# Kernel tuning notes

Measured on AMD Instinct MI355X. Metric: run time of the kernel, lower is better.

The kernel has to match this reference:

```python
import jax, jax.numpy as jnp
import numpy as np

KH, KW = 5, 5
STRIDE = 1
OUT_CH = 32
IN_CH = 3

def setup_inputs() -> dict:
    key = jax.random.key(0)
    x = jax.random.uniform(key, (16, IN_CH, 128, 128), dtype=jnp.float32)
    # reset_parameters: linspace(1, 0, out_channels) repeated over 3 channels
    rgb_weight = jnp.repeat(jnp.linspace(1.0, 0.0, OUT_CH, dtype=jnp.float32)[:, None], IN_CH, axis=1)
    return {"x": x, "rgb_weight": rgb_weight}

def _window_sum(x, kh, kw, s):
    # sum over each (kh, kw) VALID window per channel -> (B, C, oh, ow)
    return jax.lax.reduce_window(x, 0.0, jax.lax.add,
                                 (1, 1, kh, kw), (1, 1, s, s), 'VALID')

def reference(x, rgb_weight):
    kh, kw, s = KH, KW, STRIDE
    K = float(kh * kw)
    s1 = _window_sum(x, kh, kw, s)          # sum x   over window, (B,C,oh,ow)
    s2 = _window_sum(x * x, kh, kw, s)      # sum x^2 over window, (B,C,oh,ow)
    wT = rgb_weight.T                        # (C, O)
    # ||window - w*ones||^2 = S2 - 2*w*S1 + K*w^2 ; per-channel L2 dist summed over channels
    inner = (s2[:, :, None] - 2.0 * wT[None, :, :, None, None] * s1[:, :, None]
             + K * (wT * wT)[None, :, :, None, None])     # (B,C,O,oh,ow)
    dist = jnp.sqrt(jnp.maximum(inner, 0.0)).sum(axis=1)  # (B,O,oh,ow)
    # torch.std(dist) per pixel: unbiased std over all B*O entries of that pixel's dist matrix
    B, O = dist.shape[0], dist.shape[1]
    n = B * O
    mean = dist.mean(axis=(0, 1), keepdims=True)
    std = jnp.sqrt(((dist - mean) ** 2).sum(axis=(0, 1), keepdims=True) / (n - 1))
    # gaussian RBF
    return jnp.exp(-0.5 * (dist / std) ** 2)
```

## Files before the change

### kernel.cpp

```cpp
#include <hip/hip_runtime.h>
#include <math.h>

#define BB 16
#define CC 3
#define OO 32
#define HH 128
#define WW 128
#define OH 124
#define OW 124
#define NPIX (OH * OW)
#define NG   (NPIX / 4)
#define GW   (OW / 4)
#define KF 25.0f

#define TPB  256
#define NBLK (NG / 4)

typedef float vfloat4 __attribute__((ext_vector_type(4)));

#if defined(__has_builtin)
#if __has_builtin(__builtin_amdgcn_sqrtf)
#define FSQRT(x) __builtin_amdgcn_sqrtf(x)
#else
#define FSQRT(x) sqrtf(x)
#endif
#else
#define FSQRT(x) sqrtf(x)
#endif

__global__ __launch_bounds__(TPB, 4)
void fused_one(const float* __restrict__ x,
               const float* __restrict__ wgt,
               float* __restrict__ out) {
    __shared__ float  sS1[BB * CC][17];
    __shared__ float  sS2[BB * CC][17];
    __shared__ float  sPS[BB * 4][17];
    __shared__ float  sPQ[BB * 4][17];
    __shared__ float  sW[OO * CC];
    __shared__ float  sInv[16];
    __shared__ double sRm[16][4];
    __shared__ double sRq[16][4];

    const int t = threadIdx.x;

    const int orig = blockIdx.x;
    const int xcd  = orig & 7;
    const int loc  = orig >> 3;
    const int chunk = ((xcd == 0) ? 0 : 121 + (xcd - 1) * 120) + loc;
    const int g0 = chunk * 4;

    if (t < OO * CC) sW[t] = wgt[t];
    if (t < BB * CC * 4) {
        int bc = t >> 2;
        int p4 = t & 3;
        int g  = g0 + p4;
        int i  = g / GW;
        int j0 = (g % GW) * 4;
        const float* img = x + (size_t)bc * (HH * WW);
        float S1[4] = {0, 0, 0, 0}, S2[4] = {0, 0, 0, 0};
#pragma unroll
        for (int di = 0; di < 5; ++di) {
            const float4* rp = reinterpret_cast<const float4*>(img + (i + di) * WW + j0);
            float4 lo = rp[0], hi = rp[1];
            float v[8] = {lo.x, lo.y, lo.z, lo.w, hi.x, hi.y, hi.z, hi.w};
            float q[8];
#pragma unroll
            for (int k = 0; k < 8; ++k) q[k] = v[k] * v[k];
            float r  = v[0] + v[1] + v[2] + v[3] + v[4];
            float rq = q[0] + q[1] + q[2] + q[3] + q[4];
            S1[0] += r;  S2[0] += rq;
#pragma unroll
            for (int u = 1; u < 4; ++u) {
                r  += v[u + 4] - v[u - 1];
                rq += q[u + 4] - q[u - 1];
                S1[u] += r;  S2[u] += rq;
            }
        }
#pragma unroll
        for (int u = 0; u < 4; ++u) {
            sS1[bc][p4 * 4 + u] = S1[u];
            sS2[bc][p4 * 4 + u] = S2[u];
        }
    }
    __syncthreads();

    const int b  = t >> 4;
    const int og = (t >> 2) & 3;
    const int p4 = t & 3;

    float S1c[CC][4], S2c[CC][4];
#pragma unroll
    for (int c = 0; c < CC; ++c) {
#pragma unroll
        for (int u = 0; u < 4; ++u) {
            S1c[c][u] = sS1[b * CC + c][p4 * 4 + u];
            S2c[c][u] = sS2[b * CC + c][p4 * 4 + u];
        }
    }

    float dist[8][4];
    float sum[4] = {0, 0, 0, 0}, sq[4] = {0, 0, 0, 0};
#pragma unroll
    for (int oo = 0; oo < 8; ++oo) {
        int o = og * 8 + oo;
        float d[4] = {0, 0, 0, 0};
#pragma unroll
        for (int c = 0; c < CC; ++c) {
            float w  = sW[o * CC + c];
            float tw = 2.0f * w;
            float kw = KF * w * w;
#pragma unroll
            for (int u = 0; u < 4; ++u) {
                float inner = S2c[c][u] - tw * S1c[c][u] + kw;
                d[u] += FSQRT(fmaxf(inner, 0.0f));
            }
        }
#pragma unroll
        for (int u = 0; u < 4; ++u) {
            dist[oo][u] = d[u];
            sum[u] += d[u];
            sq[u]  += d[u] * d[u];
        }
    }
#pragma unroll
    for (int u = 0; u < 4; ++u) {
        sPS[b * 4 + og][p4 * 4 + u] = sum[u];
        sPQ[b * 4 + og][p4 * 4 + u] = sq[u];
    }
    __syncthreads();

    if (t < 64) {
        int pix = t >> 2;
        int seg = t & 3;
        double sm = 0.0, sQ = 0.0;
#pragma unroll
        for (int k = 0; k < 16; ++k) {
            sm += (double)sPS[seg * 16 + k][pix];
            sQ += (double)sPQ[seg * 16 + k][pix];
        }
        sRm[pix][seg] = sm;
        sRq[pix][seg] = sQ;
    }
    __syncthreads();
    if (t < 16) {
        double sm = sRm[t][0] + sRm[t][1] + sRm[t][2] + sRm[t][3];
        double sQ = sRq[t][0] + sRq[t][1] + sRq[t][2] + sRq[t][3];
        const double n = (double)(BB * OO);
        double mean = sm / n;
        double var = (sQ - n * mean * mean) / (n - 1.0);
        if (var < 0.0) var = 0.0;
        sInv[t] = (float)(1.0 / sqrt(var));
    }
    __syncthreads();

    float isd[4];
#pragma unroll
    for (int u = 0; u < 4; ++u) isd[u] = sInv[p4 * 4 + u];
    const size_t pixbase = (size_t)(g0 + p4) * 4;

#pragma unroll
    for (int oo = 0; oo < 8; ++oo) {
        int o = og * 8 + oo;
        vfloat4 r;
        float z0 = dist[oo][0] * isd[0]; r.x = __expf(-0.5f * z0 * z0);
        float z1 = dist[oo][1] * isd[1]; r.y = __expf(-0.5f * z1 * z1);
        float z2 = dist[oo][2] * isd[2]; r.z = __expf(-0.5f * z2 * z2);
        float z3 = dist[oo][3] * isd[3]; r.w = __expf(-0.5f * z3 * z3);
        __builtin_nontemporal_store(r,
            reinterpret_cast<vfloat4*>(&out[(size_t)(b * OO + o) * NPIX + pixbase]));
    }
}

extern "C" void kernel_launch(void* const* d_in, const int* in_sizes, int n_in,
                              void* d_out, int out_size, void* d_ws, size_t ws_size,
                              hipStream_t stream) {
    const float* x   = (const float*)d_in[0];
    const float* wgt = (const float*)d_in[1];
    float* out = (float*)d_out;

    fused_one<<<NBLK, TPB, 0, stream>>>(x, wgt, out);
}
```

Baseline: 17.61 us.

## Double pixels per block, fold exp scaling into exp2, drop nontemporal stores

Each block now covers 32 pixels with 512 threads instead of 16 pixels with 256, so there are about half as many blocks. The XCD chunk mapping is rebuilt for the new count, and out-of-range groups are zero-filled and their stores skipped. The Gaussian is now computed as exp2 of minus z squared, with the constant sqrt(0.5*log2 e) folded into the inverse std, which saves a multiply per element. Output stores change from nontemporal to plain float4 stores. This gives fewer blocks with more work each, at the cost of lower occupancy per CU and some tail imbalance.

```diff
diff --git a/kernel.cpp b/kernel.cpp
--- a/kernel.cpp
+++ b/kernel.cpp
@@ -13,10 +13,8 @@
 #define GW   (OW / 4)
 #define KF 25.0f
 
-#define TPB  256
-#define NBLK (NG / 4)
-
-typedef float vfloat4 __attribute__((ext_vector_type(4)));
+#define TPB  512
+#define NBLK 481
 
 #if defined(__has_builtin)
 #if __has_builtin(__builtin_amdgcn_sqrtf)
@@ -28,65 +26,84 @@
 #define FSQRT(x) sqrtf(x)
 #endif
 
-__global__ __launch_bounds__(TPB, 4)
+#define K2EXP 0.84932180f
+#if defined(__has_builtin)
+#if __has_builtin(__builtin_amdgcn_exp2f)
+#define FEXP2(x) __builtin_amdgcn_exp2f(x)
+#else
+#define FEXP2(x) exp2f(x)
+#endif
+#else
+#define FEXP2(x) exp2f(x)
+#endif
+
+__global__ __launch_bounds__(TPB, 2)
 void fused_one(const float* __restrict__ x,
                const float* __restrict__ wgt,
                float* __restrict__ out) {
-    __shared__ float  sS1[BB * CC][17];
-    __shared__ float  sS2[BB * CC][17];
-    __shared__ float  sPS[BB * 4][17];
-    __shared__ float  sPQ[BB * 4][17];
+    __shared__ float  sS1[BB * CC][33];
+    __shared__ float  sS2[BB * CC][33];
+    __shared__ float  sPS[BB * 4][33];
+    __shared__ float  sPQ[BB * 4][33];
     __shared__ float  sW[OO * CC];
-    __shared__ float  sInv[16];
-    __shared__ double sRm[16][4];
-    __shared__ double sRq[16][4];
+    __shared__ float  sInv[32];
+    __shared__ double sRm[32][4];
+    __shared__ double sRq[32][4];
 
     const int t = threadIdx.x;
 
     const int orig = blockIdx.x;
     const int xcd  = orig & 7;
     const int loc  = orig >> 3;
-    const int chunk = ((xcd == 0) ? 0 : 121 + (xcd - 1) * 120) + loc;
-    const int g0 = chunk * 4;
+    const int chunk = ((xcd == 0) ? 0 : 61 + (xcd - 1) * 60) + loc;
+    const int g0 = chunk * 8;
 
     if (t < OO * CC) sW[t] = wgt[t];
-    if (t < BB * CC * 4) {
-        int bc = t >> 2;
-        int p4 = t & 3;
+    if (t < BB * CC * 8) {
+        int bc = t >> 3;
+        int p4 = t & 7;
         int g  = g0 + p4;
-        int i  = g / GW;
-        int j0 = (g % GW) * 4;
-        const float* img = x + (size_t)bc * (HH * WW);
-        float S1[4] = {0, 0, 0, 0}, S2[4] = {0, 0, 0, 0};
-#pragma unroll
-        for (int di = 0; di < 5; ++di) {
-            const float4* rp = reinterpret_cast<const float4*>(img + (i + di) * WW + j0);
-            float4 lo = rp[0], hi = rp[1];
-            float v[8] = {lo.x, lo.y, lo.z, lo.w, hi.x, hi.y, hi.z, hi.w};
-            float q[8];
-#pragma unroll
-            for (int k = 0; k < 8; ++k) q[k] = v[k] * v[k];
-            float r  = v[0] + v[1] + v[2] + v[3] + v[4];
-            float rq = q[0] + q[1] + q[2] + q[3] + q[4];
-            S1[0] += r;  S2[0] += rq;
-#pragma unroll
-            for (int u = 1; u < 4; ++u) {
-                r  += v[u + 4] - v[u - 1];
-                rq += q[u + 4] - q[u - 1];
-                S1[u] += r;  S2[u] += rq;
-            }
-        }
-#pragma unroll
-        for (int u = 0; u < 4; ++u) {
-            sS1[bc][p4 * 4 + u] = S1[u];
-            sS2[bc][p4 * 4 + u] = S2[u];
-        }
-    }
-    __syncthreads();
-
-    const int b  = t >> 4;
-    const int og = (t >> 2) & 3;
-    const int p4 = t & 3;
+        if (g < NG) {
+            int i  = g / GW;
+            int j0 = (g % GW) * 4;
+            const float* img = x + (size_t)bc * (HH * WW);
+            float S1[4] = {0, 0, 0, 0}, S2[4] = {0, 0, 0, 0};
+#pragma unroll
+            for (int di = 0; di < 5; ++di) {
+                const float4* rp = reinterpret_cast<const float4*>(img + (i + di) * WW + j0);
+                float4 lo = rp[0], hi = rp[1];
+                float v[8] = {lo.x, lo.y, lo.z, lo.w, hi.x, hi.y, hi.z, hi.w};
+                float q[8];
+#pragma unroll
+                for (int k = 0; k < 8; ++k) q[k] = v[k] * v[k];
+                float r  = v[0] + v[1] + v[2] + v[3] + v[4];
+                float rq = q[0] + q[1] + q[2] + q[3] + q[4];
+                S1[0] += r;  S2[0] += rq;
+#pragma unroll
+                for (int u = 1; u < 4; ++u) {
+                    r  += v[u + 4] - v[u - 1];
+                    rq += q[u + 4] - q[u - 1];
+                    S1[u] += r;  S2[u] += rq;
+                }
+            }
+#pragma unroll
+            for (int u = 0; u < 4; ++u) {
+                sS1[bc][p4 * 4 + u] = S1[u];
+                sS2[bc][p4 * 4 + u] = S2[u];
+            }
+        } else {
+#pragma unroll
+            for (int u = 0; u < 4; ++u) {
+                sS1[bc][p4 * 4 + u] = 0.0f;
+                sS2[bc][p4 * 4 + u] = 0.0f;
+            }
+        }
+    }
+    __syncthreads();
+
+    const int b  = t >> 5;
+    const int og = (t >> 3) & 3;
+    const int p4 = t & 7;
 
     float S1c[CC][4], S2c[CC][4];
 #pragma unroll
@@ -129,7 +146,7 @@
     }
     __syncthreads();
 
-    if (t < 64) {
+    if (t < 128) {
         int pix = t >> 2;
         int seg = t & 3;
         double sm = 0.0, sQ = 0.0;
@@ -142,32 +159,34 @@
         sRq[pix][seg] = sQ;
     }
     __syncthreads();
-    if (t < 16) {
+    if (t < 32) {
         double sm = sRm[t][0] + sRm[t][1] + sRm[t][2] + sRm[t][3];
         double sQ = sRq[t][0] + sRq[t][1] + sRq[t][2] + sRq[t][3];
         const double n = (double)(BB * OO);
         double mean = sm / n;
         double var = (sQ - n * mean * mean) / (n - 1.0);
         if (var < 0.0) var = 0.0;
-        sInv[t] = (float)(1.0 / sqrt(var));
+        sInv[t] = (float)(K2EXP / sqrt(var));
     }
     __syncthreads();
 
     float isd[4];
 #pragma unroll
     for (int u = 0; u < 4; ++u) isd[u] = sInv[p4 * 4 + u];
+    const bool valid = (g0 + p4) < NG;
     const size_t pixbase = (size_t)(g0 + p4) * 4;
 
 #pragma unroll
     for (int oo = 0; oo < 8; ++oo) {
         int o = og * 8 + oo;
-        vfloat4 r;
-        float z0 = dist[oo][0] * isd[0]; r.x = __expf(-0.5f * z0 * z0);
-        float z1 = dist[oo][1] * isd[1]; r.y = __expf(-0.5f * z1 * z1);
-        float z2 = dist[oo][2] * isd[2]; r.z = __expf(-0.5f * z2 * z2);
-        float z3 = dist[oo][3] * isd[3]; r.w = __expf(-0.5f * z3 * z3);
-        __builtin_nontemporal_store(r,
-            reinterpret_cast<vfloat4*>(&out[(size_t)(b * OO + o) * NPIX + pixbase]));
+        float4 r;
+        float z0 = dist[oo][0] * isd[0]; r.x = FEXP2(-(z0 * z0));
+        float z1 = dist[oo][1] * isd[1]; r.y = FEXP2(-(z1 * z1));
+        float z2 = dist[oo][2] * isd[2]; r.z = FEXP2(-(z2 * z2));
+        float z3 = dist[oo][3] * isd[3]; r.w = FEXP2(-(z3 * z3));
+        if (valid) {
+            *reinterpret_cast<float4*>(&out[(size_t)(b * OO + o) * NPIX + pixbase]) = r;
+        }
     }
 }
 
```

Result: slower. 18.35 us (+4.2%).
